# Kernel optimization log

Hardware: AMD Instinct MI355X
Metric: run time of the kernel (lower is better)

Reference implementation:

```python
import jax, jax.numpy as jnp
import numpy as np


def _gru(x, h0, Wi, Wh, bi, bh):
    """PyTorch-equations GRU. x: (T,B,D), Wi: (3H,D), Wh: (3H,H). Returns (ys, hT)."""
    xW = jnp.einsum('tbd,gd->tbg', x, Wi) + bi  # (T,B,3H) precomputed input proj
    def step(h, xw):
        hw = h @ Wh.T + bh
        xr, xz, xn = jnp.split(xw, 3, axis=-1)
        hr, hz, hn = jnp.split(hw, 3, axis=-1)
        r = jax.nn.sigmoid(xr + hr)
        z = jax.nn.sigmoid(xz + hz)
        n = jnp.tanh(xn + r * hn)
        h_new = (1.0 - z) * n + z * h
        return h_new, h_new
    hT, ys = jax.lax.scan(step, h0, xW)
    return ys, hT


def _bigru(x, WiF, WhF, biF, bhF, WiB, WhB, biB, bhB):
    B = x.shape[1]
    H = WhF.shape[1]
    h0 = jnp.zeros((B, H), x.dtype)
    yf, hf = _gru(x, h0, WiF, WhF, biF, bhF)
    yb, hb = _gru(x[::-1], h0, WiB, WhB, biB, bhB)
    return jnp.concatenate([yf, yb[::-1]], axis=-1), jnp.stack([hf, hb], axis=0)


def _ln(x, g, b, eps=1e-5):
    mu = x.mean(-1, keepdims=True)
    var = ((x - mu) ** 2).mean(-1, keepdims=True)
    return (x - mu) * jax.lax.rsqrt(var + eps) * g + b


def _forward(tokens, emb,
             s_WiF, s_WhF, s_biF, s_bhF, s_lnF_g, s_lnF_b,
             s_Wi_f, s_Wh_f, s_bi_f, s_bh_f, s_Wi_b, s_Wh_b, s_bi_b, s_bh_b,
             s_ln_g, s_ln_b, s_linW, s_linb,
             d_WiF, d_WhF, d_biF, d_bhF, d_lnF_g, d_lnF_b,
             d_Wi_f, d_Wh_f, d_bi_f, d_bh_f, d_Wi_b, d_Wh_b, d_bi_b, d_bh_b,
             d_ln_g, d_ln_b, out_W, out_b):
    S, T, B = tokens.shape
    H = s_WhF.shape[1]
    # sentence loop is batch-independent -> fold sentences into batch
    x = emb[tokens]                                  # (S,T,B,E)
    x = x.transpose(1, 0, 2, 3).reshape(T, S * B, -1)  # (T, S*B, E)
    h0 = jnp.zeros((S * B, H), x.dtype)
    y, _ = _gru(x, h0, s_WiF, s_WhF, s_biF, s_bhF)
    y = _ln(y, s_lnF_g, s_lnF_b)
    y, _ = _bigru(y, s_Wi_f, s_Wh_f, s_bi_f, s_bh_f, s_Wi_b, s_Wh_b, s_bi_b, s_bh_b)
    y = _ln(y, s_ln_g, s_ln_b)
    y = jnp.tanh(y @ s_linW.T + s_linb)              # (T, S*B, H)
    store = y.mean(axis=0).reshape(S, B, H)          # per-sentence mean-pooled cell
    # document-level encoder over sentence sequence
    h0d = jnp.zeros((B, H), x.dtype)
    y, _ = _gru(store, h0d, d_WiF, d_WhF, d_biF, d_bhF)
    y = _ln(y, d_lnF_g, d_lnF_b)
    y, _ = _bigru(y, d_Wi_f, d_Wh_f, d_bi_f, d_bh_f, d_Wi_b, d_Wh_b, d_bi_b, d_bh_b)
    y = _ln(y, d_ln_g, d_ln_b)
    return jax.nn.sigmoid(y @ out_W.T + out_b)       # (S, B, O)


def setup_inputs() -> dict:
    V, E, H, O = 32000, 256, 256, 2
    S, T, B = 96, 32, 32
    keys = iter(jax.random.split(jax.random.key(0), 64))
    def g(shape, scale=0.06):
        return jax.random.normal(next(keys), shape, jnp.float32) * scale
    inp = {}
    inp['tokens'] = jax.random.randint(next(keys), (S, T, B), 0, V)
    inp['emb'] = g((V, E), 0.1)
    # sentence encoder: uni GRU (E->H), LN(H), bi GRU (H->H), LN(2H), linear 2H->H
    inp['s_WiF'] = g((3 * H, E)); inp['s_WhF'] = g((3 * H, H))
    inp['s_biF'] = jnp.zeros((3 * H,)); inp['s_bhF'] = jnp.zeros((3 * H,))
    inp['s_lnF_g'] = jnp.ones((H,)); inp['s_lnF_b'] = jnp.zeros((H,))
    inp['s_Wi_f'] = g((3 * H, H)); inp['s_Wh_f'] = g((3 * H, H))
    inp['s_bi_f'] = jnp.zeros((3 * H,)); inp['s_bh_f'] = jnp.zeros((3 * H,))
    inp['s_Wi_b'] = g((3 * H, H)); inp['s_Wh_b'] = g((3 * H, H))
    inp['s_bi_b'] = jnp.zeros((3 * H,)); inp['s_bh_b'] = jnp.zeros((3 * H,))
    inp['s_ln_g'] = jnp.ones((2 * H,)); inp['s_ln_b'] = jnp.zeros((2 * H,))
    inp['s_linW'] = g((H, 2 * H)); inp['s_linb'] = jnp.zeros((H,))
    # document encoder: uni GRU (H->H), LN(H), bi GRU (H->H), LN(2H)
    inp['d_WiF'] = g((3 * H, H)); inp['d_WhF'] = g((3 * H, H))
    inp['d_biF'] = jnp.zeros((3 * H,)); inp['d_bhF'] = jnp.zeros((3 * H,))
    inp['d_lnF_g'] = jnp.ones((H,)); inp['d_lnF_b'] = jnp.zeros((H,))
    inp['d_Wi_f'] = g((3 * H, H)); inp['d_Wh_f'] = g((3 * H, H))
    inp['d_bi_f'] = jnp.zeros((3 * H,)); inp['d_bh_f'] = jnp.zeros((3 * H,))
    inp['d_Wi_b'] = g((3 * H, H)); inp['d_Wh_b'] = g((3 * H, H))
    inp['d_bi_b'] = jnp.zeros((3 * H,)); inp['d_bh_b'] = jnp.zeros((3 * H,))
    inp['d_ln_g'] = jnp.ones((2 * H,)); inp['d_ln_b'] = jnp.zeros((2 * H,))
    inp['out_W'] = g((O, 2 * H)); inp['out_b'] = jnp.zeros((O,))
    return inp


def reference(tokens, emb,
              s_WiF, s_WhF, s_biF, s_bhF, s_lnF_g, s_lnF_b,
              s_Wi_f, s_Wh_f, s_bi_f, s_bh_f, s_Wi_b, s_Wh_b, s_bi_b, s_bh_b,
              s_ln_g, s_ln_b, s_linW, s_linb,
              d_WiF, d_WhF, d_biF, d_bhF, d_lnF_g, d_lnF_b,
              d_Wi_f, d_Wh_f, d_bi_f, d_bh_f, d_Wi_b, d_Wh_b, d_bi_b, d_bh_b,
              d_ln_g, d_ln_b, out_W, out_b):
    return _forward(tokens, emb,
                    s_WiF, s_WhF, s_biF, s_bhF, s_lnF_g, s_lnF_b,
                    s_Wi_f, s_Wh_f, s_bi_f, s_bh_f, s_Wi_b, s_Wh_b, s_bi_b, s_bh_b,
                    s_ln_g, s_ln_b, s_linW, s_linb,
                    d_WiF, d_WhF, d_biF, d_bhF, d_lnF_g, d_lnF_b,
                    d_Wi_f, d_Wh_f, d_bi_f, d_bh_f, d_Wi_b, d_Wh_b, d_bi_b, d_bh_b,
                    d_ln_g, d_ln_b, out_W, out_b)
```

## Files before the change

kernel.cpp:

```cpp
#include <hip/hip_runtime.h>


typedef __bf16 bf16;
typedef __bf16 bf16x8 __attribute__((ext_vector_type(8)));
typedef __bf16 bf16x4 __attribute__((ext_vector_type(4)));
typedef float  f32x4  __attribute__((ext_vector_type(4)));

static __device__ __forceinline__ f32x4 mfma16(bf16x8 a, bf16x8 b, f32x4 c) {
  return __builtin_amdgcn_mfma_f32_16x16x32_bf16(a, b, c, 0, 0, 0);
}
static __device__ __forceinline__ float sigm(float x) { return 1.f / (1.f + __expf(-x)); }
static __device__ __forceinline__ bf16x8 asbf(f32x4 v) {
  union { f32x4 f; bf16x8 b; } u; u.f = v; return u.b;
}
static __device__ __forceinline__ void wg_barrier() {
  asm volatile("s_waitcnt lgkmcnt(0)" ::: "memory");
  __builtin_amdgcn_s_barrier();
  __builtin_amdgcn_sched_barrier(0);
}
static __device__ __forceinline__ void gload16(const bf16* g, bf16* l) {
  __builtin_amdgcn_global_load_lds(
      (const __attribute__((address_space(1))) void*)g,
      (__attribute__((address_space(3))) void*)l, 16, 0, 0);
}

__global__ __launch_bounds__(256) void cvt_bf16(
    const float* __restrict__ s, bf16* __restrict__ d, int n4)
{
  int i = blockIdx.x * 256 + threadIdx.x;
  if (i < n4) {
    float4 v = ((const float4*)s)[i];
    bf16x4 o;
    o[0] = (bf16)v.x; o[1] = (bf16)v.y; o[2] = (bf16)v.z; o[3] = (bf16)v.w;
    ((bf16x4*)d)[i] = o;
  }
}

__global__ __launch_bounds__(256) void conv13(
    const float* s0, const float* s1, const float* s2, const float* s3,
    const float* s4, const float* s5, const float* s6, const float* s7,
    const float* s8, const float* s9, const float* s10, const float* s11,
    const float* s12, bf16* __restrict__ dst)
{
  const float* srcs[13] = {s0,s1,s2,s3,s4,s5,s6,s7,s8,s9,s10,s11,s12};
  int m = blockIdx.y;
  int n4 = (m == 12) ? 32768 : 49152;
  int i = blockIdx.x * 256 + threadIdx.x;
  if (i >= n4) return;
  float4 v = ((const float4*)srcs[m])[i];
  bf16x4 o;
  o[0] = (bf16)v.x; o[1] = (bf16)v.y; o[2] = (bf16)v.z; o[3] = (bf16)v.w;
  ((bf16x4*)(dst + (size_t)m * 196608))[i] = o;
}

__global__ __launch_bounds__(256) void prep_bias(
    const float* b0i, const float* b0h, const float* b1i, const float* b1h,
    const float* b2i, const float* b2h, const float* b3i, const float* b3h,
    const float* b4i, const float* b4h, const float* b5i, const float* b5h,
    float* __restrict__ out)
{
  const float* bis[6] = {b0i,b1i,b2i,b3i,b4i,b5i};
  const float* bhs[6] = {b0h,b1h,b2h,b3h,b4h,b5h};
  int g = blockIdx.y;
  int i = blockIdx.x * 256 + threadIdx.x;
  if (i < 768)
    out[g * 768 + i] = bis[g][i] + (i < 512 ? bhs[g][i] : 0.f);
}

__global__ __launch_bounds__(256) void xw_gemm(
    const bf16* __restrict__ X,
    const bf16* __restrict__ W0, const float* __restrict__ b0, bf16* __restrict__ o0,
    const bf16* __restrict__ W1, const float* __restrict__ b1, bf16* __restrict__ o1)
{
  const bf16* W = blockIdx.y ? W1 : W0;
  const float* bias = blockIdx.y ? b1 : b0;
  bf16* out = blockIdx.y ? o1 : o0;
  int wave = (int)blockIdx.x * 4 + (threadIdx.x >> 6);
  int g64 = wave / 48, ct = wave - g64 * 48;
  int lane = threadIdx.x & 63;
  int r16 = lane & 15, g4 = lane >> 4;
  const bf16* wp = W + (size_t)(ct * 16 + r16) * 256;
  const bf16* xb = X + ((size_t)g64 * 64 + r16) * 256;
  f32x4 a0 = {0,0,0,0}, a1 = {0,0,0,0}, a2 = {0,0,0,0}, a3 = {0,0,0,0};
#pragma unroll
  for (int kk = 0; kk < 8; kk++) {
    int k0 = kk * 32 + g4 * 8;
    bf16x8 wf = *(const bf16x8*)(wp + k0);
    a0 = mfma16(*(const bf16x8*)(xb + k0), wf, a0);
    a1 = mfma16(*(const bf16x8*)(xb + 4096 + k0), wf, a1);
    a2 = mfma16(*(const bf16x8*)(xb + 8192 + k0), wf, a2);
    a3 = mfma16(*(const bf16x8*)(xb + 12288 + k0), wf, a3);
  }
  float bv = bias[ct * 16 + r16];
#pragma unroll
  for (int rt = 0; rt < 4; rt++) {
    f32x4 ac = rt == 0 ? a0 : rt == 1 ? a1 : rt == 2 ? a2 : a3;
#pragma unroll
    for (int j = 0; j < 4; j++)
      out[(size_t)(g64 * 64 + rt * 16 + g4 * 4 + j) * 768 + ct * 16 + r16] = (bf16)(ac[j] + bv);
  }
}

__global__ __launch_bounds__(256) void xw_gather_gemm(
    const int* __restrict__ tok, const bf16* __restrict__ embb,
    const bf16* __restrict__ W, const float* __restrict__ bias,
    bf16* __restrict__ out, int c)
{
  int t = blockIdx.y;
  int wave = (int)blockIdx.x * 4 + (threadIdx.x >> 6);
  int g64 = wave / 48, ct = wave - g64 * 48;
  int lane = threadIdx.x & 63;
  int r16 = lane & 15, g4 = lane >> 4;
  const bf16* wp = W + (size_t)(ct * 16 + r16) * 256;
  const bf16* ap[4];
#pragma unroll
  for (int rt = 0; rt < 4; rt++) {
    int n = g64 * 64 + rt * 16 + r16;
    int tk = tok[((n >> 5) << 10) + (t << 5) + (n & 31)];
    ap[rt] = embb + (size_t)tk * 256;
  }
  f32x4 a0 = {0,0,0,0}, a1 = {0,0,0,0}, a2 = {0,0,0,0}, a3 = {0,0,0,0};
#pragma unroll
  for (int kk = 0; kk < 8; kk++) {
    int k0 = kk * 32 + g4 * 8;
    bf16x8 wf = *(const bf16x8*)(wp + k0);
    a0 = mfma16(*(const bf16x8*)(ap[0] + k0), wf, a0);
    a1 = mfma16(*(const bf16x8*)(ap[1] + k0), wf, a1);
    a2 = mfma16(*(const bf16x8*)(ap[2] + k0), wf, a2);
    a3 = mfma16(*(const bf16x8*)(ap[3] + k0), wf, a3);
  }
  float bv = bias[ct * 16 + r16];
#pragma unroll
  for (int rt = 0; rt < 4; rt++) {
    f32x4 ac = rt == 0 ? a0 : rt == 1 ? a1 : rt == 2 ? a2 : a3;
#pragma unroll
    for (int j = 0; j < 4; j++)
      out[((size_t)t * c + g64 * 64 + rt * 16 + g4 * 4 + j) * 768 + ct * 16 + r16] = (bf16)(ac[j] + bv);
  }
}

__global__ __launch_bounds__(512)
__attribute__((amdgpu_waves_per_eu(1, 2)))
void pgru(
    const bf16* __restrict__ xw0, const bf16* __restrict__ Wh0, const float* __restrict__ bh0,
    const bf16* __restrict__ xw1, const bf16* __restrict__ Wh1, const float* __restrict__ bh1,
    bf16* __restrict__ yout0, bf16* __restrict__ yout1, int ostride,
    const float* __restrict__ lng, const float* __restrict__ lnb,
    int steps, int Mtot, int rev0, int rev1)
{
  int dir = blockIdx.y;
  const bf16*  xw = dir ? xw1 : xw0;
  const bf16*  Wh = dir ? Wh1 : Wh0;
  const float* bh = dir ? bh1 : bh0;
  bf16* yout = dir ? yout1 : yout0;
  int rev = dir ? rev1 : rev0;

  __shared__ __align__(16) bf16 hbuf[16][264];
  __shared__ __align__(16) bf16 xbuf[2][8][3][16][32];
  __shared__ bf16 ldspad[12544];

  int tid = threadIdx.x;
  int w = tid >> 6, lane = tid & 63, r16 = lane & 15, g4 = lane >> 4;
  int rowbase = (int)blockIdx.x * 16;
  int c0 = w * 32 + r16, c1 = c0 + 16;
  if (steps == 0) ldspad[tid] = (bf16)0.f;

  for (int i2 = tid; i2 < 528; i2 += 512) ((bf16x8*)hbuf)[i2] = (bf16x8){};

  f32x4 wr0[8], wz0[8], wn0[8], wr1[8], wz1[8], wn1[8];
  {
    const bf16* W0 = Wh + (size_t)c0 * 256;
    const bf16* W1 = Wh + (size_t)c1 * 256;
#pragma unroll
    for (int kk = 0; kk < 8; kk++) {
      int k0 = kk * 32 + g4 * 8;
      wr0[kk] = *(const f32x4*)(W0 + k0);          asm volatile("" : "+v"(wr0[kk]));
      wz0[kk] = *(const f32x4*)(W0 + 65536 + k0);  asm volatile("" : "+v"(wz0[kk]));
      wn0[kk] = *(const f32x4*)(W0 + 131072 + k0); asm volatile("" : "+v"(wn0[kk]));
      wr1[kk] = *(const f32x4*)(W1 + k0);          asm volatile("" : "+v"(wr1[kk]));
      wz1[kk] = *(const f32x4*)(W1 + 65536 + k0);  asm volatile("" : "+v"(wz1[kk]));
      wn1[kk] = *(const f32x4*)(W1 + 131072 + k0); asm volatile("" : "+v"(wn1[kk]));
    }
  }
  float bhn0 = bh[c0 + 512], bhn1 = bh[c1 + 512];

  auto stage = [&](int b, int st) {
    int row = rowbase + (lane >> 2);
    const bf16* s = xw + ((size_t)st * Mtot + row) * 768 + w * 32 + (lane & 3) * 8;
    gload16(s,       &xbuf[b][w][0][0][0]);
    gload16(s + 256, &xbuf[b][w][1][0][0]);
    gload16(s + 512, &xbuf[b][w][2][0][0]);
  };
  stage(0, rev ? steps - 1 : 0);
  wg_barrier();

  for (int i = 0; i < steps; i++) {
    int cur = i & 1;
    int st = rev ? steps - 1 - i : i;
    if (i + 1 < steps) {
      stage(cur ^ 1, rev ? steps - 2 - i : i + 1);
      asm volatile("s_waitcnt vmcnt(3)" ::: "memory");
    } else {
      asm volatile("s_waitcnt vmcnt(0)" ::: "memory");
    }
    __builtin_amdgcn_sched_barrier(0);

    float hn0[4], hn1[4];
    {
      f32x4 a0 = {0,0,0,0}, a1 = {0,0,0,0}, a2 = {0,0,0,0};
#pragma unroll
      for (int kk = 0; kk < 8; kk++) {
        bf16x8 a = *(const bf16x8*)&hbuf[r16][kk * 32 + g4 * 8];
        a0 = mfma16(a, asbf(wr0[kk]), a0);
        a1 = mfma16(a, asbf(wz0[kk]), a1);
        a2 = mfma16(a, asbf(wn0[kk]), a2);
      }
#pragma unroll
      for (int j = 0; j < 4; j++) {
        int m = g4 * 4 + j;
        float r = sigm((float)xbuf[cur][w][0][m][r16] + a0[j]);
        float z = sigm((float)xbuf[cur][w][1][m][r16] + a1[j]);
        float n = tanhf((float)xbuf[cur][w][2][m][r16] + r * (a2[j] + bhn0));
        hn0[j] = (1.f - z) * n + z * (float)hbuf[m][c0];
      }
    }
    {
      f32x4 a0 = {0,0,0,0}, a1 = {0,0,0,0}, a2 = {0,0,0,0};
#pragma unroll
      for (int kk = 0; kk < 8; kk++) {
        bf16x8 a = *(const bf16x8*)&hbuf[r16][kk * 32 + g4 * 8];
        a0 = mfma16(a, asbf(wr1[kk]), a0);
        a1 = mfma16(a, asbf(wz1[kk]), a1);
        a2 = mfma16(a, asbf(wn1[kk]), a2);
      }
#pragma unroll
      for (int j = 0; j < 4; j++) {
        int m = g4 * 4 + j;
        float r = sigm((float)xbuf[cur][w][0][m][r16 + 16] + a0[j]);
        float z = sigm((float)xbuf[cur][w][1][m][r16 + 16] + a1[j]);
        float n = tanhf((float)xbuf[cur][w][2][m][r16 + 16] + r * (a2[j] + bhn1));
        hn1[j] = (1.f - z) * n + z * (float)hbuf[m][c1];
      }
    }
    wg_barrier();
#pragma unroll
    for (int j = 0; j < 4; j++) {
      int m = g4 * 4 + j;
      hbuf[m][c0] = (bf16)hn0[j];
      hbuf[m][c1] = (bf16)hn1[j];
    }
    if (!lng) {
#pragma unroll
      for (int j = 0; j < 4; j++) {
        size_t ro = ((size_t)st * Mtot + rowbase + g4 * 4 + j) * ostride;
        yout[ro + c0] = (bf16)hn0[j];
        yout[ro + c1] = (bf16)hn1[j];
      }
    }
    wg_barrier();
    if (lng) {
#pragma unroll
      for (int rr = 0; rr < 2; rr++) {
        int r = w * 2 + rr;
        bf16x4 v4 = *(const bf16x4*)&hbuf[r][lane * 4];
        float v[4]; float sm = 0.f, sq = 0.f;
#pragma unroll
        for (int j = 0; j < 4; j++) { v[j] = (float)v4[j]; sm += v[j]; sq += v[j] * v[j]; }
        for (int msk = 32; msk; msk >>= 1) { sm += __shfl_xor(sm, msk); sq += __shfl_xor(sq, msk); }
        float mu  = sm * (1.f / 256.f);
        float var = sq * (1.f / 256.f) - mu * mu;
        float inv = rsqrtf(fmaxf(var, 0.f) + 1e-5f);
        bf16x4 o;
#pragma unroll
        for (int j = 0; j < 4; j++)
          o[j] = (bf16)((v[j] - mu) * inv * lng[lane * 4 + j] + lnb[lane * 4 + j]);
        *(bf16x4*)&yout[((size_t)st * Mtot + rowbase + r) * ostride + lane * 4] = o;
      }
    }
  }
}

__global__ __launch_bounds__(256) void sent_tail_part(
    const bf16* __restrict__ hf, const bf16* __restrict__ hb,
    const float* __restrict__ gam, const float* __restrict__ bet,
    const bf16* __restrict__ W, const float* __restrict__ bias,
    float* __restrict__ part, int c)
{
  int wave = threadIdx.x >> 6;
  int lane = threadIdx.x & 63;
  int r16 = lane & 15, g4 = lane >> 4;
  int r0 = (int)blockIdx.x << 4;
  int tg = blockIdx.y;
  size_t rowoff = (size_t)(r0 + r16) * 256;

  f32x4 ms0 = {0,0,0,0}, ms1 = {0,0,0,0}, ms2 = {0,0,0,0}, ms3 = {0,0,0,0};

  for (int tt = 0; tt < 4; tt++) {
    int t = tg * 4 + tt;
    const bf16* pf = hf + (size_t)t * c * 256 + rowoff;
    const bf16* pb = hb + (size_t)t * c * 256 + rowoff;
    bf16x8 xv[16];
    float s = 0.f, sq = 0.f;
#pragma unroll
    for (int kk = 0; kk < 16; kk++) {
      int k0 = kk * 32 + g4 * 8;
      xv[kk] = (kk < 8) ? *(const bf16x8*)(pf + k0) : *(const bf16x8*)(pb + k0 - 256);
#pragma unroll
      for (int j = 0; j < 8; j++) { float f = (float)xv[kk][j]; s += f; sq += f * f; }
    }
    s  += __shfl_xor(s, 16);  s  += __shfl_xor(s, 32);
    sq += __shfl_xor(sq, 16); sq += __shfl_xor(sq, 32);
    float mu  = s * (1.f / 512.f);
    float var = sq * (1.f / 512.f) - mu * mu;
    float inv = rsqrtf(fmaxf(var, 0.f) + 1e-5f);
#pragma unroll
    for (int kk = 0; kk < 16; kk++) {
      int k0 = kk * 32 + g4 * 8;
      float ga[8], be[8];
      *(float4*)(ga)     = *(const float4*)(gam + k0);
      *(float4*)(ga + 4) = *(const float4*)(gam + k0 + 4);
      *(float4*)(be)     = *(const float4*)(bet + k0);
      *(float4*)(be + 4) = *(const float4*)(bet + k0 + 4);
#pragma unroll
      for (int j = 0; j < 8; j++)
        xv[kk][j] = (bf16)(((float)xv[kk][j] - mu) * inv * ga[j] + be[j]);
    }
#pragma unroll
    for (int tc = 0; tc < 4; tc++) {
      int cj = wave * 64 + tc * 16;
      const bf16* wp = W + (size_t)(cj + r16) * 512;
      f32x4 acc = {0,0,0,0};
#pragma unroll
      for (int kk = 0; kk < 16; kk++)
        acc = mfma16(xv[kk], *(const bf16x8*)(wp + kk * 32 + g4 * 8), acc);
      float bb = bias[cj + r16];
      f32x4* msp = (tc == 0) ? &ms0 : (tc == 1) ? &ms1 : (tc == 2) ? &ms2 : &ms3;
#pragma unroll
      for (int j = 0; j < 4; j++) (*msp)[j] += tanhf(acc[j] + bb);
    }
  }
#pragma unroll
  for (int tc = 0; tc < 4; tc++) {
    int cj = wave * 64 + tc * 16;
    f32x4 ms = (tc == 0) ? ms0 : (tc == 1) ? ms1 : (tc == 2) ? ms2 : ms3;
#pragma unroll
    for (int j = 0; j < 4; j++)
      part[((size_t)tg * c + r0 + g4 * 4 + j) * 256 + cj + r16] = ms[j];
  }
}

__global__ __launch_bounds__(256) void tail_reduce(
    const float* __restrict__ part, bf16* __restrict__ out, int c)
{
  int idx = blockIdx.x * 256 + threadIdx.x;
  float s = 0.f;
#pragma unroll
  for (int g = 0; g < 8; g++) s += part[(size_t)g * c * 256 + idx];
  out[idx] = (bf16)(s * 0.03125f);
}

__global__ __launch_bounds__(256) void ln_out_head(
    const bf16* __restrict__ X, const float* __restrict__ lng, const float* __restrict__ lnb,
    const float* __restrict__ W, const float* __restrict__ bias, float* __restrict__ out)
{
  int w = threadIdx.x >> 6, lane = threadIdx.x & 63;
  int row = (int)blockIdx.x * 4 + w;
  bf16x8 v8 = *(const bf16x8*)&X[(size_t)row * 512 + lane * 8];
  float v[8]; float sm = 0.f, sq = 0.f;
#pragma unroll
  for (int j = 0; j < 8; j++) { v[j] = (float)v8[j]; sm += v[j]; sq += v[j] * v[j]; }
  for (int msk = 32; msk; msk >>= 1) { sm += __shfl_xor(sm, msk); sq += __shfl_xor(sq, msk); }
  float mu  = sm * (1.f / 512.f);
  float var = sq * (1.f / 512.f) - mu * mu;
  float inv = rsqrtf(fmaxf(var, 0.f) + 1e-5f);
  float a0 = 0.f, a1 = 0.f;
  int base = lane * 8;
#pragma unroll
  for (int j = 0; j < 8; j++) {
    float y = (v[j] - mu) * inv * lng[base + j] + lnb[base + j];
    a0 += y * W[base + j];
    a1 += y * W[512 + base + j];
  }
  for (int msk = 32; msk; msk >>= 1) { a0 += __shfl_xor(a0, msk); a1 += __shfl_xor(a1, msk); }
  if (lane == 0) {
    out[(size_t)row * 2 + 0] = sigm(a0 + bias[0]);
    out[(size_t)row * 2 + 1] = sigm(a1 + bias[1]);
  }
}

extern "C" void kernel_launch(void* const* d_in, const int* in_sizes, int n_in,
                              void* d_out, int out_size, void* d_ws, size_t ws_size,
                              hipStream_t stream)
{
  (void)in_sizes; (void)n_in; (void)out_size;
  const int*   tokens = (const int*)d_in[0];
  const float* emb    = (const float*)d_in[1];
  auto fp = [&](int i) { return (const float*)d_in[i]; };
  const float *s_WiF = fp(2),  *s_WhF = fp(3),  *s_biF = fp(4),  *s_bhF = fp(5);
  const float *s_lnF_g = fp(6), *s_lnF_b = fp(7);
  const float *s_Wi_f = fp(8),  *s_Wh_f = fp(9),  *s_bi_f = fp(10), *s_bh_f = fp(11);
  const float *s_Wi_b = fp(12), *s_Wh_b = fp(13), *s_bi_b = fp(14), *s_bh_b = fp(15);
  const float *s_ln_g = fp(16), *s_ln_b = fp(17), *s_linW = fp(18), *s_linb = fp(19);
  const float *dWiF = fp(20), *dWhF = fp(21), *dbiF = fp(22), *dbhF = fp(23);
  const float *d_lnF_g = fp(24), *d_lnF_b = fp(25);
  const float *dWi_f = fp(26), *dWh_f = fp(27), *dbi_f = fp(28), *dbh_f = fp(29);
  const float *dWi_b = fp(30), *dWh_b = fp(31), *dbi_b = fp(32), *dbh_b = fp(33);
  const float *d_ln_g = fp(34), *d_ln_b = fp(35), *out_W = fp(36), *out_b = fp(37);

  const int T = 32, S = 96;
  const int GW = 196608;

  bf16* wc = (bf16*)d_ws;
  bf16 *c_sWiF = wc,         *c_sWhF = wc + GW;
  bf16 *c_sWif = wc + 2*GW,  *c_sWhf = wc + 3*GW;
  bf16 *c_sWib = wc + 4*GW,  *c_sWhb = wc + 5*GW;
  bf16 *c_dWiF = wc + 6*GW,  *c_dWhF = wc + 7*GW;
  bf16 *c_dWif = wc + 8*GW,  *c_dWhf = wc + 9*GW;
  bf16 *c_dWib = wc + 10*GW, *c_dWhb = wc + 11*GW;
  bf16 *c_linW = wc + 12*GW;
  const size_t WB = (size_t)(12 * GW + 131072) * 2;
  bf16* embb = (bf16*)((char*)d_ws + WB);
  const size_t EB = (size_t)32000 * 256 * 2;
  float* bmod = (float*)((char*)d_ws + WB + EB);
  const size_t BMB = 6 * 768 * 4;

  conv13<<<dim3(192, 13), 256, 0, stream>>>(
      s_WiF, s_WhF, s_Wi_f, s_Wh_f, s_Wi_b, s_Wh_b,
      dWiF, dWhF, dWi_f, dWh_f, dWi_b, dWh_b, s_linW, wc);
  cvt_bf16<<<8000, 256, 0, stream>>>(emb, embb, 2048000);
  prep_bias<<<dim3(3, 6), 256, 0, stream>>>(
      s_biF, s_bhF, s_bi_f, s_bh_f, s_bi_b, s_bh_b,
      dbiF, dbhF, dbi_f, dbh_f, dbi_b, dbh_b, bmod);
  const float *bm_sF = bmod, *bm_sf = bmod + 768, *bm_sb = bmod + 1536;
  const float *bm_dF = bmod + 2304, *bm_df = bmod + 3072, *bm_db = bmod + 3840;

  char* ws = (char*)d_ws + WB + EB + BMB;
  bf16* store = (bf16*)ws;
  bf16* yd1ln = store + (size_t)3072 * 256;
  bf16* ybid  = yd1ln + (size_t)3072 * 256;
  bf16* xw_u  = ybid  + (size_t)3072 * 512;
  bf16* xwdf  = xw_u  + (size_t)3072 * 768;
  bf16* xwdb  = xwdf  + (size_t)3072 * 768;
  const size_t fixedB = WB + EB + BMB
      + ((size_t)3072 * 256 * 2 + (size_t)3072 * 512 + (size_t)3 * 3072 * 768) * 2;

  int c = 3072;
  while (c > 192 && fixedB + (size_t)98304 * c > ws_size) c >>= 1;
  char* cb = (char*)d_ws + fixedB;
  bf16*  xw   = (bf16*)cb;
  bf16*  y1ln = (bf16*)(cb + (size_t)49152 * c);
  bf16*  hf   = (bf16*)(cb + (size_t)65536 * c);
  bf16*  hb   = (bf16*)(cb + (size_t)81920 * c);
  float* part = (float*)cb;

  for (int base = 0; base < 3072; base += c) {
    const int* tkb = tokens + (size_t)base * 32;
    xw_gather_gemm<<<dim3((c / 64) * 12, T), 256, 0, stream>>>(
        tkb, embb, c_sWiF, bm_sF, xw, c);
    pgru<<<dim3(c / 16, 1), 512, 0, stream>>>(
        xw, c_sWhF, s_bhF, nullptr, nullptr, nullptr,
        y1ln, nullptr, 256, s_lnF_g, s_lnF_b, T, c, 0, 0);
    xw_gemm<<<dim3((T * c / 64) * 12, 1), 256, 0, stream>>>(
        y1ln, c_sWif, bm_sf, xw, nullptr, nullptr, nullptr);
    pgru<<<dim3(c / 16, 1), 512, 0, stream>>>(
        xw, c_sWhf, s_bh_f, nullptr, nullptr, nullptr,
        hf, nullptr, 256, nullptr, nullptr, T, c, 0, 0);
    xw_gemm<<<dim3((T * c / 64) * 12, 1), 256, 0, stream>>>(
        y1ln, c_sWib, bm_sb, xw, nullptr, nullptr, nullptr);
    pgru<<<dim3(c / 16, 1), 512, 0, stream>>>(
        xw, c_sWhb, s_bh_b, nullptr, nullptr, nullptr,
        hb, nullptr, 256, nullptr, nullptr, T, c, 1, 0);
    sent_tail_part<<<dim3(c / 16, 8), 256, 0, stream>>>(
        hf, hb, s_ln_g, s_ln_b, c_linW, s_linb, part, c);
    tail_reduce<<<c, 256, 0, stream>>>(part, store + (size_t)base * 256, c);
  }

  xw_gemm<<<dim3((3072 / 64) * 12, 1), 256, 0, stream>>>(
      store, c_dWiF, bm_dF, xw_u, nullptr, nullptr, nullptr);
  pgru<<<dim3(2, 1), 512, 0, stream>>>(
      xw_u, c_dWhF, dbhF, nullptr, nullptr, nullptr,
      yd1ln, nullptr, 256, d_lnF_g, d_lnF_b, S, 32, 0, 0);
  xw_gemm<<<dim3((3072 / 64) * 12, 2), 256, 0, stream>>>(
      yd1ln, c_dWif, bm_df, xwdf, c_dWib, bm_db, xwdb);
  pgru<<<dim3(2, 2), 512, 0, stream>>>(
      xwdf, c_dWhf, dbh_f, xwdb, c_dWhb, dbh_b,
      ybid, ybid + 256, 512, nullptr, nullptr, S, 32, 0, 1);
  ln_out_head<<<768, 256, 0, stream>>>(ybid, d_ln_g, d_ln_b, out_W, out_b,
                                       (float*)d_out);
}
```

Before: 3.635 ms.

## Split GRU recurrence across 16 waves with one column tile per wave

```diff
diff --git a/kernel.cpp b/kernel.cpp
--- a/kernel.cpp
+++ b/kernel.cpp
@@ -139,8 +139,8 @@
   }
 }
 
-__global__ __launch_bounds__(512)
-__attribute__((amdgpu_waves_per_eu(1, 2)))
+__global__ __launch_bounds__(1024)
+__attribute__((amdgpu_waves_per_eu(4, 4)))
 void pgru(
     const bf16* __restrict__ xw0, const bf16* __restrict__ Wh0, const float* __restrict__ bh0,
     const bf16* __restrict__ xw1, const bf16* __restrict__ Wh1, const float* __restrict__ bh1,
@@ -156,126 +156,92 @@
   int rev = dir ? rev1 : rev0;
 
   __shared__ __align__(16) bf16 hbuf[16][264];
-  __shared__ __align__(16) bf16 xbuf[2][8][3][16][32];
-  __shared__ bf16 ldspad[12544];
+  __shared__ __align__(16) bf16 xbuf[2][16][3][16][16];
 
   int tid = threadIdx.x;
   int w = tid >> 6, lane = tid & 63, r16 = lane & 15, g4 = lane >> 4;
   int rowbase = (int)blockIdx.x * 16;
-  int c0 = w * 32 + r16, c1 = c0 + 16;
-  if (steps == 0) ldspad[tid] = (bf16)0.f;
-
-  for (int i2 = tid; i2 < 528; i2 += 512) ((bf16x8*)hbuf)[i2] = (bf16x8){};
-
-  f32x4 wr0[8], wz0[8], wn0[8], wr1[8], wz1[8], wn1[8];
+  int c0 = w * 16 + r16;
+
+  for (int i2 = tid; i2 < 528; i2 += 1024) ((bf16x8*)hbuf)[i2] = (bf16x8){};
+
+  f32x4 wr[8], wz[8], wn[8];
   {
     const bf16* W0 = Wh + (size_t)c0 * 256;
-    const bf16* W1 = Wh + (size_t)c1 * 256;
 #pragma unroll
     for (int kk = 0; kk < 8; kk++) {
       int k0 = kk * 32 + g4 * 8;
-      wr0[kk] = *(const f32x4*)(W0 + k0);          asm volatile("" : "+v"(wr0[kk]));
-      wz0[kk] = *(const f32x4*)(W0 + 65536 + k0);  asm volatile("" : "+v"(wz0[kk]));
-      wn0[kk] = *(const f32x4*)(W0 + 131072 + k0); asm volatile("" : "+v"(wn0[kk]));
-      wr1[kk] = *(const f32x4*)(W1 + k0);          asm volatile("" : "+v"(wr1[kk]));
-      wz1[kk] = *(const f32x4*)(W1 + 65536 + k0);  asm volatile("" : "+v"(wz1[kk]));
-      wn1[kk] = *(const f32x4*)(W1 + 131072 + k0); asm volatile("" : "+v"(wn1[kk]));
-    }
-  }
-  float bhn0 = bh[c0 + 512], bhn1 = bh[c1 + 512];
-
+      wr[kk] = *(const f32x4*)(W0 + k0);          asm volatile("" : "+v"(wr[kk]));
+      wz[kk] = *(const f32x4*)(W0 + 65536 + k0);  asm volatile("" : "+v"(wz[kk]));
+      wn[kk] = *(const f32x4*)(W0 + 131072 + k0); asm volatile("" : "+v"(wn[kk]));
+    }
+  }
+  float bhn0 = bh[c0 + 512];
+
+  int m_ = (lane & 31) >> 1;
+  int k_ = (lane & 1) * 8;
+  int gsel = (lane >> 5) * 256;
   auto stage = [&](int b, int st) {
-    int row = rowbase + (lane >> 2);
-    const bf16* s = xw + ((size_t)st * Mtot + row) * 768 + w * 32 + (lane & 3) * 8;
-    gload16(s,       &xbuf[b][w][0][0][0]);
-    gload16(s + 256, &xbuf[b][w][1][0][0]);
-    gload16(s + 512, &xbuf[b][w][2][0][0]);
+    const bf16* s1 = xw + ((size_t)st * Mtot + rowbase + m_) * 768 + gsel + w * 16 + k_;
+    gload16(s1,       &xbuf[b][w][0][0][0]);
+    gload16(s1 + 256, &xbuf[b][w][1][0][0]);
   };
   stage(0, rev ? steps - 1 : 0);
-  wg_barrier();
 
   for (int i = 0; i < steps; i++) {
     int cur = i & 1;
     int st = rev ? steps - 1 - i : i;
     if (i + 1 < steps) {
       stage(cur ^ 1, rev ? steps - 2 - i : i + 1);
-      asm volatile("s_waitcnt vmcnt(3)" ::: "memory");
+      asm volatile("s_waitcnt vmcnt(2)" ::: "memory");
     } else {
       asm volatile("s_waitcnt vmcnt(0)" ::: "memory");
     }
     __builtin_amdgcn_sched_barrier(0);
-
-    float hn0[4], hn1[4];
-    {
-      f32x4 a0 = {0,0,0,0}, a1 = {0,0,0,0}, a2 = {0,0,0,0};
-#pragma unroll
-      for (int kk = 0; kk < 8; kk++) {
-        bf16x8 a = *(const bf16x8*)&hbuf[r16][kk * 32 + g4 * 8];
-        a0 = mfma16(a, asbf(wr0[kk]), a0);
-        a1 = mfma16(a, asbf(wz0[kk]), a1);
-        a2 = mfma16(a, asbf(wn0[kk]), a2);
-      }
-#pragma unroll
-      for (int j = 0; j < 4; j++) {
-        int m = g4 * 4 + j;
-        float r = sigm((float)xbuf[cur][w][0][m][r16] + a0[j]);
-        float z = sigm((float)xbuf[cur][w][1][m][r16] + a1[j]);
-        float n = tanhf((float)xbuf[cur][w][2][m][r16] + r * (a2[j] + bhn0));
-        hn0[j] = (1.f - z) * n + z * (float)hbuf[m][c0];
-      }
-    }
-    {
-      f32x4 a0 = {0,0,0,0}, a1 = {0,0,0,0}, a2 = {0,0,0,0};
-#pragma unroll
-      for (int kk = 0; kk < 8; kk++) {
-        bf16x8 a = *(const bf16x8*)&hbuf[r16][kk * 32 + g4 * 8];
-        a0 = mfma16(a, asbf(wr1[kk]), a0);
-        a1 = mfma16(a, asbf(wz1[kk]), a1);
-        a2 = mfma16(a, asbf(wn1[kk]), a2);
-      }
-#pragma unroll
-      for (int j = 0; j < 4; j++) {
-        int m = g4 * 4 + j;
-        float r = sigm((float)xbuf[cur][w][0][m][r16 + 16] + a0[j]);
-        float z = sigm((float)xbuf[cur][w][1][m][r16 + 16] + a1[j]);
-        float n = tanhf((float)xbuf[cur][w][2][m][r16 + 16] + r * (a2[j] + bhn1));
-        hn1[j] = (1.f - z) * n + z * (float)hbuf[m][c1];
-      }
-    }
     wg_barrier();
+
+    f32x4 a0 = {0,0,0,0}, a1 = {0,0,0,0}, a2 = {0,0,0,0};
+#pragma unroll
+    for (int kk = 0; kk < 8; kk++) {
+      bf16x8 a = *(const bf16x8*)&hbuf[r16][kk * 32 + g4 * 8];
+      a0 = mfma16(a, asbf(wr[kk]), a0);
+      a1 = mfma16(a, asbf(wz[kk]), a1);
+      a2 = mfma16(a, asbf(wn[kk]), a2);
+    }
+    float hn[4];
 #pragma unroll
     for (int j = 0; j < 4; j++) {
       int m = g4 * 4 + j;
-      hbuf[m][c0] = (bf16)hn0[j];
-      hbuf[m][c1] = (bf16)hn1[j];
-    }
+      float r = sigm((float)xbuf[cur][w][0][m][r16] + a0[j]);
+      float z = sigm((float)xbuf[cur][w][1][m][r16] + a1[j]);
+      float n = tanhf((float)xbuf[cur][w][2][m][r16] + r * (a2[j] + bhn0));
+      hn[j] = (1.f - z) * n + z * (float)hbuf[m][c0];
+    }
+    wg_barrier();
+#pragma unroll
+    for (int j = 0; j < 4; j++)
+      hbuf[g4 * 4 + j][c0] = (bf16)hn[j];
     if (!lng) {
 #pragma unroll
       for (int j = 0; j < 4; j++) {
         size_t ro = ((size_t)st * Mtot + rowbase + g4 * 4 + j) * ostride;
-        yout[ro + c0] = (bf16)hn0[j];
-        yout[ro + c1] = (bf16)hn1[j];
+        yout[ro + c0] = (bf16)hn[j];
       }
-    }
-    wg_barrier();
-    if (lng) {
-#pragma unroll
-      for (int rr = 0; rr < 2; rr++) {
-        int r = w * 2 + rr;
-        bf16x4 v4 = *(const bf16x4*)&hbuf[r][lane * 4];
-        float v[4]; float sm = 0.f, sq = 0.f;
-#pragma unroll
-        for (int j = 0; j < 4; j++) { v[j] = (float)v4[j]; sm += v[j]; sq += v[j] * v[j]; }
-        for (int msk = 32; msk; msk >>= 1) { sm += __shfl_xor(sm, msk); sq += __shfl_xor(sq, msk); }
-        float mu  = sm * (1.f / 256.f);
-        float var = sq * (1.f / 256.f) - mu * mu;
-        float inv = rsqrtf(fmaxf(var, 0.f) + 1e-5f);
-        bf16x4 o;
-#pragma unroll
-        for (int j = 0; j < 4; j++)
-          o[j] = (bf16)((v[j] - mu) * inv * lng[lane * 4 + j] + lnb[lane * 4 + j]);
-        *(bf16x4*)&yout[((size_t)st * Mtot + rowbase + r) * ostride + lane * 4] = o;
-      }
+    } else {
+      wg_barrier();
+      bf16x4 v4 = *(const bf16x4*)&hbuf[w][lane * 4];
+      float v[4]; float sm = 0.f, sq = 0.f;
+#pragma unroll
+      for (int j = 0; j < 4; j++) { v[j] = (float)v4[j]; sm += v[j]; sq += v[j] * v[j]; }
+      for (int msk = 32; msk; msk >>= 1) { sm += __shfl_xor(sm, msk); sq += __shfl_xor(sq, msk); }
+      float mu  = sm * (1.f / 256.f);
+      float var = sq * (1.f / 256.f) - mu * mu;
+      float inv = rsqrtf(fmaxf(var, 0.f) + 1e-5f);
+      bf16x4 o;
+#pragma unroll
+      for (int j = 0; j < 4; j++)
+        o[j] = (bf16)((v[j] - mu) * inv * lng[lane * 4 + j] + lnb[lane * 4 + j]);
+      *(bf16x4*)&yout[((size_t)st * Mtot + rowbase + w) * ostride + lane * 4] = o;
     }
   }
 }
@@ -457,17 +423,17 @@
     const int* tkb = tokens + (size_t)base * 32;
     xw_gather_gemm<<<dim3((c / 64) * 12, T), 256, 0, stream>>>(
         tkb, embb, c_sWiF, bm_sF, xw, c);
-    pgru<<<dim3(c / 16, 1), 512, 0, stream>>>(
+    pgru<<<dim3(c / 16, 1), 1024, 0, stream>>>(
         xw, c_sWhF, s_bhF, nullptr, nullptr, nullptr,
         y1ln, nullptr, 256, s_lnF_g, s_lnF_b, T, c, 0, 0);
     xw_gemm<<<dim3((T * c / 64) * 12, 1), 256, 0, stream>>>(
         y1ln, c_sWif, bm_sf, xw, nullptr, nullptr, nullptr);
-    pgru<<<dim3(c / 16, 1), 512, 0, stream>>>(
+    pgru<<<dim3(c / 16, 1), 1024, 0, stream>>>(
         xw, c_sWhf, s_bh_f, nullptr, nullptr, nullptr,
         hf, nullptr, 256, nullptr, nullptr, T, c, 0, 0);
     xw_gemm<<<dim3((T * c / 64) * 12, 1), 256, 0, stream>>>(
         y1ln, c_sWib, bm_sb, xw, nullptr, nullptr, nullptr);
-    pgru<<<dim3(c / 16, 1), 512, 0, stream>>>(
+    pgru<<<dim3(c / 16, 1), 1024, 0, stream>>>(
         xw, c_sWhb, s_bh_b, nullptr, nullptr, nullptr,
         hb, nullptr, 256, nullptr, nullptr, T, c, 1, 0);
     sent_tail_part<<<dim3(c / 16, 8), 256, 0, stream>>>(
@@ -477,12 +443,12 @@
 
   xw_gemm<<<dim3((3072 / 64) * 12, 1), 256, 0, stream>>>(
       store, c_dWiF, bm_dF, xw_u, nullptr, nullptr, nullptr);
-  pgru<<<dim3(2, 1), 512, 0, stream>>>(
+  pgru<<<dim3(2, 1), 1024, 0, stream>>>(
       xw_u, c_dWhF, dbhF, nullptr, nullptr, nullptr,
       yd1ln, nullptr, 256, d_lnF_g, d_lnF_b, S, 32, 0, 0);
   xw_gemm<<<dim3((3072 / 64) * 12, 2), 256, 0, stream>>>(
       yd1ln, c_dWif, bm_df, xwdf, c_dWib, bm_db, xwdb);
-  pgru<<<dim3(2, 2), 512, 0, stream>>>(
+  pgru<<<dim3(2, 2), 1024, 0, stream>>>(
       xwdf, c_dWhf, dbh_f, xwdb, c_dWhb, dbh_b,
       ybid, ybid + 256, 512, nullptr, nullptr, S, 32, 0, 1);
   ln_out_head<<<768, 256, 0, stream>>>(ybid, d_ln_g, d_ln_b, out_W, out_b,
```

Result: no change. 3.632 ms (-0.1%).
